# Performance work log

Hardware: AMD Instinct MI355X
Metric: run time of the kernel (lower is better)

The kernel has to match this reference:

```python
import jax, jax.numpy as jnp
import numpy as np
import math

B, T, D_MODEL, N_HEADS = 4, 2048, 1024, 16
HEAD_DIM = D_MODEL // N_HEADS


def setup_inputs() -> dict:
    key = jax.random.key(0)
    k1, k2, k3 = jax.random.split(key, 3)
    x = jax.random.normal(k1, (B, T, D_MODEL), dtype=jnp.float32)
    # torch Linear weight layout: [out_features, in_features]
    w_qkv = jax.random.normal(k2, (3 * D_MODEL, D_MODEL), dtype=jnp.float32) * (1.0 / math.sqrt(D_MODEL))
    w_out = jax.random.normal(k3, (D_MODEL, D_MODEL), dtype=jnp.float32) * (1.0 / math.sqrt(D_MODEL))
    return {"x": x, "w_qkv": w_qkv, "w_out": w_out}


def reference(x, w_qkv, w_out):
    b, t, c = x.shape
    h, d = N_HEADS, HEAD_DIM
    # qkv projection: (B,T,3C) -> (3,B,H,T,D)
    qkv = jnp.einsum('btc,fc->btf', x, w_qkv)
    qkv = qkv.reshape(b, t, 3, h, d).transpose(2, 0, 3, 1, 4)
    q, k, v = qkv[0], qkv[1], qkv[2]
    scale = 1.0 / math.sqrt(d)
    # full O(T^2) attention scores, causal masked
    scores = jnp.einsum('bhqd,bhkd->bhqk', q, k) * scale
    causal = jnp.tril(jnp.ones((t, t), dtype=bool))
    scores = jnp.where(causal[None, None, :, :], scores, jnp.float32(-jnp.inf))
    attn = jax.nn.softmax(scores, axis=-1)
    out = jnp.einsum('bhqk,bhkd->bhqd', attn, v)  # (B,H,T,D)
    out = out.transpose(0, 2, 1, 3).reshape(b, t, c)
    out = jnp.einsum('btc,oc->bto', out, w_out)
    return out
```

## Files before the change

### kernel.cpp

```cpp
#include <hip/hip_runtime.h>
#include <hip/hip_bf16.h>

#define T_SEQ 2048
#define BATCH 4
#define NH    16
#define DM    1024
#define HD    64

typedef __attribute__((ext_vector_type(4))) float  f32x4;
typedef __attribute__((ext_vector_type(8))) short  s16x8;
typedef __attribute__((ext_vector_type(4))) short  s16x4;
typedef __attribute__((ext_vector_type(4))) unsigned short u16x4;

__device__ __forceinline__ unsigned short f2b(float f) {
  union { float f; unsigned u; } v; v.f = f;
  unsigned u = v.u;
  unsigned r = 0x7fffu + ((u >> 16) & 1u);
  u += r;
  return (unsigned short)(u >> 16);
}

__device__ __forceinline__ f32x4 mfma16(s16x8 a, s16x8 b, f32x4 c) {
  return __builtin_amdgcn_mfma_f32_16x16x32_bf16(a, b, c, 0, 0, 0);
}

__device__ __forceinline__ float exp2_fast(float x) {
  float r; asm("v_exp_f32 %0, %1" : "=v"(r) : "v"(x)); return r;
}

__device__ __forceinline__ unsigned cvt_pk_bf16(float lo, float hi) {
  unsigned r; asm("v_cvt_pk_bf16_f32 %0, %1, %2" : "=v"(r) : "v"(lo), "v"(hi)); return r;
}

__global__ void cvt_all(const float* __restrict__ x, const float* __restrict__ wq,
                        const float* __restrict__ wo,
                        unsigned short* __restrict__ xb, unsigned short* __restrict__ wqb,
                        unsigned short* __restrict__ wob) {
  const int N4X = (BATCH * T_SEQ * DM) / 4;
  const int N4Q = (3 * DM * DM) / 4;
  const int N4O = (DM * DM) / 4;
  const int N4QSCALED = (DM * DM) / 4;
  int i = blockIdx.x * blockDim.x + threadIdx.x;
  int stride = gridDim.x * blockDim.x;
  for (int j = i; j < N4X + N4Q + N4O; j += stride) {
    const float* src; unsigned short* dst; int k; float scale = 1.f;
    if (j < N4X) { src = x; dst = xb; k = j; }
    else if (j < N4X + N4Q) {
      k = j - N4X; src = wq; dst = wqb;
      if (k < N4QSCALED) scale = 0.18033688011112042f;
    } else { k = j - N4X - N4Q; src = wo; dst = wob; }
    f32x4 v = ((const f32x4*)src)[k];
    s16x4 o;
    o.x = (short)f2b(v.x * scale); o.y = (short)f2b(v.y * scale);
    o.z = (short)f2b(v.z * scale); o.w = (short)f2b(v.w * scale);
    ((s16x4*)dst)[k] = o;
  }
}

template<int OUT_F32>
__global__ __launch_bounds__(256)
void gemm_bt(const unsigned short* __restrict__ A,
             const unsigned short* __restrict__ B,
             void* __restrict__ C, int M, int N, int K) {
  __shared__ unsigned short As[128 * 32];
  __shared__ unsigned short Bs[128 * 32];
  const int tid  = threadIdx.x;
  const int lane = tid & 63;
  const int w    = tid >> 6;
  const int wr   = w >> 1, wc = w & 1;
  const int lr   = lane & 15, g = lane >> 4;

  const int gx  = gridDim.x, nwg = gx * gridDim.y;
  const int bid = blockIdx.y * gx + blockIdx.x;
  const int cpx = nwg >> 3;
  const int b2  = (bid & 7) * cpx + (bid >> 3);
  const int row0 = (b2 % gx) * 128;
  const int col0 = (b2 / gx) * 128;

  const int srow = w * 16 + (lane >> 2);
  const int scol = (lane & 3) * 8;

  f32x4 acc[4][4] = {};

  for (int kt = 0; kt < K; kt += 32) {
    __syncthreads();
#pragma unroll
    for (int s = 0; s < 2; ++s) {
      const unsigned short* srcA = A + (size_t)(row0 + s * 64 + srow) * K + kt + scol;
      __builtin_amdgcn_global_load_lds((const void*)srcA, (void*)&As[(s * 64 + w * 16) * 32], 16, 0, 0);
      const unsigned short* srcB = B + (size_t)(col0 + s * 64 + srow) * K + kt + scol;
      __builtin_amdgcn_global_load_lds((const void*)srcB, (void*)&Bs[(s * 64 + w * 16) * 32], 16, 0, 0);
    }
    __syncthreads();

    s16x8 af[4], bf[4];
#pragma unroll
    for (int m = 0; m < 4; ++m)
      af[m] = *(const s16x8*)&As[(wr * 64 + m * 16 + lr) * 32 + g * 8];
#pragma unroll
    for (int n = 0; n < 4; ++n)
      bf[n] = *(const s16x8*)&Bs[(wc * 64 + n * 16 + lr) * 32 + g * 8];
#pragma unroll
    for (int m = 0; m < 4; ++m)
#pragma unroll
      for (int n = 0; n < 4; ++n)
        acc[m][n] = mfma16(af[m], bf[n], acc[m][n]);
  }

#pragma unroll
  for (int m = 0; m < 4; ++m)
#pragma unroll
    for (int n = 0; n < 4; ++n)
#pragma unroll
      for (int i = 0; i < 4; ++i) {
        int row = row0 + wr * 64 + m * 16 + g * 4 + i;
        int col = col0 + wc * 64 + n * 16 + lr;
        if (OUT_F32)
          ((float*)C)[(size_t)row * N + col] = acc[m][n][i];
        else
          ((unsigned short*)C)[(size_t)row * N + col] = f2b(acc[m][n][i]);
      }
}

__global__ __launch_bounds__(512)
void attn_kernel(const unsigned short* __restrict__ qkv,
                 unsigned short* __restrict__ out) {
  __shared__ unsigned short Ks[2][64 * 64];
  __shared__ unsigned short Vt[2][64 * 72];
  __shared__ unsigned short Ps[8][16 * 72];

  const int tid  = threadIdx.x;
  const int lane = tid & 63;
  const int w    = tid >> 6;
  const int lr   = lane & 15, g = lane >> 4;
  const int bid  = blockIdx.x;
  const int bh   = bid & 63;
  const int pi   = bid >> 6;
  const int b    = bh >> 4, h = bh & 15;
  const size_t rb = (size_t)b * T_SEQ;

  const bool grpV = (tid < 256);
  const int vd0 = (tid & 7) * 8, vr0 = (tid >> 3) * 2;
  const int t2  = tid - 256;
  const int kr0 = t2 >> 3, kc0 = t2 & 7;

#pragma unroll 1
  for (int ph = 0; ph < 2; ++ph) {
    const int qt = ph ? (15 - pi) : pi;
    const int q0 = qt * 128;
    const int qr = q0 + w * 16;
    const int qq = qr + lr;
    const int nt = 2 * qt + 2;
    const int qmax = qr + 15;

    s16x8 qf[2];
    {
      const unsigned short* qp = qkv + (rb + qq) * 3072 + h * 64;
      qf[0] = *(const s16x8*)(qp + g * 8);
      qf[1] = *(const s16x8*)(qp + 32 + g * 8);
    }

    float mI = -1e30f, lI = 0.f;
    f32x4 o[4] = {};

    s16x8 pre0, pre1;
    {
      if (grpV) {
        const unsigned short* vp = &qkv[(rb + vr0) * 3072 + 2048 + h * 64 + vd0];
        pre0 = *(const s16x8*)vp;
        pre1 = *(const s16x8*)(vp + 3072);
      } else {
        const unsigned short* kp = &qkv[(rb + kr0) * 3072 + 1024 + h * 64 + kc0 * 8];
        pre0 = *(const s16x8*)kp;
        pre1 = *(const s16x8*)(kp + 32 * 3072);
      }
    }

    for (int t = 0; t < nt; ++t) {
      const int cur = t & 1;
      if (grpV) {
#pragma unroll
        for (int jj = 0; jj < 8; ++jj) {
          int d = vd0 + jj;
          int sw = ((d ^ (d >> 3)) & 7) << 4;
          unsigned val = (unsigned)(unsigned short)pre0[jj] |
                         ((unsigned)(unsigned short)pre1[jj] << 16);
          *(unsigned*)((char*)&Vt[cur][0] + d * 144 + ((vr0 * 2) ^ sw)) = val;
        }
      } else {
        *(s16x8*)((char*)&Ks[cur][0] + kr0 * 128 + ((kc0 * 16) ^ ((kr0 & 7) << 4))) = pre0;
        int kr1 = kr0 + 32;
        *(s16x8*)((char*)&Ks[cur][0] + kr1 * 128 + ((kc0 * 16) ^ ((kr1 & 7) << 4))) = pre1;
      }
      __syncthreads();

      if (t + 1 < nt) {
        const int kv0n = (t + 1) * 64;
        if (grpV) {
          const unsigned short* vp = &qkv[(rb + kv0n + vr0) * 3072 + 2048 + h * 64 + vd0];
          pre0 = *(const s16x8*)vp;
          pre1 = *(const s16x8*)(vp + 3072);
        } else {
          const unsigned short* kp = &qkv[(rb + kv0n + kr0) * 3072 + 1024 + h * 64 + kc0 * 8];
          pre0 = *(const s16x8*)kp;
          pre1 = *(const s16x8*)(kp + 32 * 3072);
        }
      }

      const int kv0 = t * 64;
      if (kv0 <= qmax) {
        f32x4 s4[4];
        __builtin_amdgcn_s_setprio(1);
#pragma unroll
        for (int kc = 0; kc < 4; ++kc) {
          int row = kc * 16 + lr;
          const char* kbase = (const char*)&Ks[cur][0] + row * 128;
          int sw = (row & 7) << 4;
          s16x8 kf0 = *(const s16x8*)(kbase + ((g * 16) ^ sw));
          s16x8 kf1 = *(const s16x8*)(kbase + ((64 + g * 16) ^ sw));
          f32x4 s = {};
          s = mfma16(kf0, qf[0], s);
          s = mfma16(kf1, qf[1], s);
          s4[kc] = s;
        }
        __builtin_amdgcn_s_setprio(0);

        if (kv0 + 63 > qr) {
#pragma unroll
          for (int kc = 0; kc < 4; ++kc)
#pragma unroll
            for (int i = 0; i < 4; ++i) {
              int key = kv0 + kc * 16 + g * 4 + i;
              if (key > qq) s4[kc][i] = -1e30f;
            }
        }

        float mx = fmaxf(fmaxf(fmaxf(s4[0][0], s4[0][1]), fmaxf(s4[0][2], s4[0][3])),
                   fmaxf(fmaxf(fmaxf(s4[1][0], s4[1][1]), fmaxf(s4[1][2], s4[1][3])),
                   fmaxf(fmaxf(fmaxf(s4[2][0], s4[2][1]), fmaxf(s4[2][2], s4[2][3])),
                         fmaxf(fmaxf(s4[3][0], s4[3][1]), fmaxf(s4[3][2], s4[3][3])))));
        mx = fmaxf(mx, __shfl_xor(mx, 16));
        mx = fmaxf(mx, __shfl_xor(mx, 32));

        const bool defer = __all(mx - mI <= 11.5f);
        float alpha;
        if (defer) {
          alpha = 1.f;
        } else {
          float mn = fmaxf(mI, mx);
          alpha = exp2_fast(mI - mn);
          mI = mn;
        }
        float rs = 0.f;
#pragma unroll
        for (int kc = 0; kc < 4; ++kc)
#pragma unroll
          for (int i = 0; i < 4; ++i) {
            float p = exp2_fast(s4[kc][i] - mI);
            s4[kc][i] = p;
            rs += p;
          }
        rs += __shfl_xor(rs, 16);
        rs += __shfl_xor(rs, 32);
        lI = lI * alpha + rs;

        {
          char* pw = (char*)&Ps[w][0] + lr * 144;
#pragma unroll
          for (int kc = 0; kc < 4; ++kc) {
            unsigned v0 = cvt_pk_bf16(s4[kc][0], s4[kc][1]);
            unsigned v1 = cvt_pk_bf16(s4[kc][2], s4[kc][3]);
            unsigned long long pv = (unsigned long long)v0 | ((unsigned long long)v1 << 32);
            *(unsigned long long*)(pw + kc * 32 + g * 8) = pv;
          }
        }

        if (!defer) {
#pragma unroll
          for (int n = 0; n < 4; ++n)
#pragma unroll
            for (int i = 0; i < 4; ++i)
              o[n][i] *= alpha;
        }

        asm volatile("s_waitcnt lgkmcnt(0)" ::: "memory");

        __builtin_amdgcn_s_setprio(1);
#pragma unroll
        for (int kk = 0; kk < 2; ++kk) {
          s16x8 pf = *(const s16x8*)((const char*)&Ps[w][0] + lr * 144 + kk * 64 + g * 16);
#pragma unroll
          for (int n = 0; n < 4; ++n) {
            int d = n * 16 + lr;
            int sw = ((d ^ (d >> 3)) & 7) << 4;
            s16x8 vf = *(const s16x8*)((const char*)&Vt[cur][0] + d * 144 + ((kk * 64 + g * 16) ^ sw));
            o[n] = mfma16(vf, pf, o[n]);
          }
        }
        __builtin_amdgcn_s_setprio(0);
      }
    }

    float rl = 1.f / lI;
#pragma unroll
    for (int n = 0; n < 4; ++n) {
      unsigned p0 = cvt_pk_bf16(o[n][0] * rl, o[n][1] * rl);
      unsigned p1 = cvt_pk_bf16(o[n][2] * rl, o[n][3] * rl);
      unsigned long long pv = (unsigned long long)p0 | ((unsigned long long)p1 << 32);
      *(unsigned long long*)&out[(rb + qq) * 1024 + h * 64 + n * 16 + g * 4] = pv;
    }
  }
}

extern "C" void kernel_launch(void* const* d_in, const int* in_sizes, int n_in,
                              void* d_out, int out_size, void* d_ws, size_t ws_size,
                              hipStream_t stream) {
  const float* x     = (const float*)d_in[0];
  const float* w_qkv = (const float*)d_in[1];
  const float* w_out = (const float*)d_in[2];

  const size_t n_x   = (size_t)BATCH * T_SEQ * DM;
  const size_t n_wq  = (size_t)3 * DM * DM;
  const size_t n_wo  = (size_t)DM * DM;
  const size_t n_qkv = (size_t)BATCH * T_SEQ * 3 * DM;
  const size_t need  = (n_x + n_wq + n_wo + n_qkv + n_x) * 2;
  if (ws_size < need) return;

  unsigned short* xb  = (unsigned short*)d_ws;
  unsigned short* wqb = xb + n_x;
  unsigned short* wob = wqb + n_wq;
  unsigned short* qkv = wob + n_wo;
  unsigned short* att = qkv + n_qkv;

  cvt_all<<<2048, 256, 0, stream>>>(x, w_qkv, w_out, xb, wqb, wob);

  gemm_bt<0><<<dim3(64, 24), 256, 0, stream>>>(xb, wqb, qkv, BATCH * T_SEQ, 3 * DM, DM);
  attn_kernel<<<512, 512, 0, stream>>>(qkv, att);
  gemm_bt<1><<<dim3(64, 8), 256, 0, stream>>>(att, wob, d_out, BATCH * T_SEQ, DM, DM);
}
```

Before: 200.2 us.

## Replace QKV projection GEMM with 256x256-tile 8-wave pipelined direct-to-LDS kernel

Adds a new bf16 GEMM kernel for the QKV projection. It uses 256x256 output tiles, 512 threads and 128KB of double-buffered LDS. Tiles are staged with global_load_lds and an XOR swizzle, and explicit waitcnt and barrier scheduling interleaves loads, LDS reads and MFMA clusters at raised priority. The goal is more data reuse per tile and memory latency hidden behind MFMA work. In exchange it uses heavy register pressure, launches only 384 workgroups (fewer than two waves across the CUs), and its exact hand-tuned waitcnt counts are fragile.

```diff
diff --git a/kernel.cpp b/kernel.cpp
--- a/kernel.cpp
+++ b/kernel.cpp
@@ -10,7 +10,6 @@
 typedef __attribute__((ext_vector_type(4))) float  f32x4;
 typedef __attribute__((ext_vector_type(8))) short  s16x8;
 typedef __attribute__((ext_vector_type(4))) short  s16x4;
-typedef __attribute__((ext_vector_type(4))) unsigned short u16x4;
 
 __device__ __forceinline__ unsigned short f2b(float f) {
   union { float f; unsigned u; } v; v.f = f;
@@ -31,6 +30,11 @@
 __device__ __forceinline__ unsigned cvt_pk_bf16(float lo, float hi) {
   unsigned r; asm("v_cvt_pk_bf16_f32 %0, %1, %2" : "=v"(r) : "v"(lo), "v"(hi)); return r;
 }
+
+#define BAR() __builtin_amdgcn_s_barrier()
+#define SCB() __builtin_amdgcn_sched_barrier(0)
+#define LGK(n) do { asm volatile("s_waitcnt lgkmcnt(" #n ")" ::: "memory"); SCB(); } while (0)
+#define VMC(n) do { asm volatile("s_waitcnt vmcnt(" #n ")" ::: "memory"); } while (0)
 
 __global__ void cvt_all(const float* __restrict__ x, const float* __restrict__ wq,
                         const float* __restrict__ wo,
@@ -57,6 +61,150 @@
   }
 }
 
+__device__ __forceinline__ void rd4(s16x8 (&d)[4], const char* base, int rbase, int cb) {
+#pragma unroll
+  for (int j = 0; j < 4; ++j)
+    d[j] = *(const s16x8*)(base + (rbase + j * 16) * 128 + cb);
+}
+
+__device__ __forceinline__ void stage_half(const unsigned short* __restrict__ Msrc,
+                                           int rt0, int kt, char* lbase, int half,
+                                           int srow8, int c2src, int c2lin, int Kd) {
+#pragma unroll
+  for (int q = 0; q < 2; ++q) {
+    int rl = half * 128 + q * 64 + srow8;
+    const char* src = (const char*)(Msrc + (size_t)(rt0 + rl) * Kd + kt) + c2src;
+    __builtin_amdgcn_global_load_lds((const void*)src, (void*)(lbase + rl * 128 + c2lin),
+                                     16, 0, 0);
+  }
+}
+
+__device__ __forceinline__ void clust(f32x4 (&acc)[8][4], const s16x8 (&a)[4],
+                                      const s16x8 (&b)[4], int mb) {
+  __builtin_amdgcn_s_setprio(1);
+#pragma unroll
+  for (int j = 0; j < 4; ++j)
+#pragma unroll
+    for (int n = 0; n < 4; ++n)
+      acc[mb + j][n] = mfma16(a[j], b[n], acc[mb + j][n]);
+  __builtin_amdgcn_s_setprio(0);
+}
+
+__global__ __launch_bounds__(512, 2)
+void gemm8p(const unsigned short* __restrict__ A, const unsigned short* __restrict__ B,
+            unsigned short* __restrict__ C, int M, int N, int K) {
+  __shared__ char smem[131072];
+  char* A0b = smem;
+  char* A1b = smem + 32768;
+  char* B0b = smem + 65536;
+  char* B1b = smem + 98304;
+
+  const int tid = threadIdx.x;
+  const int lane = tid & 63;
+  const int w = tid >> 6;
+  const int wm = w >> 2, wn = w & 3;
+  const int lr = lane & 15, g = lane >> 4;
+
+  const int gx = gridDim.x, nwg = gx * gridDim.y;
+  const int bid = blockIdx.y * gx + blockIdx.x;
+  const int cpx = nwg >> 3;
+  const int b2 = (bid & 7) * cpx + (bid >> 3);
+  const int row0 = (b2 % gx) * 256;
+  const int col0 = (b2 / gx) * 256;
+
+  const int srow8 = tid >> 3;
+  const int c2lin = (tid & 7) * 16;
+  const int swzS = ((srow8 & 4) << 3) | ((srow8 & 8) << 1);
+  const int c2src = c2lin ^ swzS;
+
+  const int swzL = ((lr & 4) << 3) | ((lr & 8) << 1);
+  const int cs0 = (g * 16) ^ swzL;
+  const int cs1 = 64 + cs0;
+  const int rAlo = wm * 128 + lr;
+  const int rAhi = rAlo + 64;
+  const int rB = wn * 64 + lr;
+
+  f32x4 acc[8][4] = {};
+  s16x8 aP[4], aQ[4], aR[4], bP[4], bQ[4];
+
+  const int NITER = K / 128;
+  const int ktLast = K - 64;
+
+  stage_half(A, row0, 0, A0b, 0, srow8, c2src, c2lin, K);
+  stage_half(A, row0, 0, A0b, 1, srow8, c2src, c2lin, K);
+  stage_half(B, col0, 0, B0b, 0, srow8, c2src, c2lin, K);
+  stage_half(B, col0, 0, B0b, 1, srow8, c2src, c2lin, K);
+  stage_half(A, row0, 64, A1b, 0, srow8, c2src, c2lin, K);
+  VMC(2);
+  BAR();
+  rd4(aP, A0b, rAlo, cs0);
+  rd4(bP, B0b, rB, cs0);
+
+  for (int it = 0; it < NITER; ++it) {
+    const int ktO = it * 128 + 64;
+    const int kt2 = min(it * 128 + 128, ktLast);
+    const int kt3 = min(it * 128 + 192, ktLast);
+
+    rd4(aQ, A0b, rAhi, cs0);
+    stage_half(B, col0, ktO, B1b, 0, srow8, c2src, c2lin, K);
+    BAR(); LGK(4);
+    clust(acc, aP, bP, 0);
+    BAR();
+    rd4(aP, A0b, rAlo, cs1);
+    rd4(aR, A0b, rAhi, cs1);
+    rd4(bQ, B0b, rB, cs1);
+    stage_half(B, col0, ktO, B1b, 1, srow8, c2src, c2lin, K);
+    BAR(); LGK(12);
+    clust(acc, aQ, bP, 4);
+    BAR();
+    stage_half(A, row0, ktO, A1b, 1, srow8, c2src, c2lin, K);
+    BAR(); LGK(0);
+    clust(acc, aP, bQ, 0);
+    BAR();
+    stage_half(A, row0, kt2, A0b, 0, srow8, c2src, c2lin, K);
+    VMC(2);
+    BAR();
+    rd4(aP, A1b, rAlo, cs0);
+    rd4(bP, B1b, rB, cs0);
+    clust(acc, aR, bQ, 4);
+    BAR();
+    rd4(aQ, A1b, rAhi, cs0);
+    stage_half(B, col0, kt2, B0b, 0, srow8, c2src, c2lin, K);
+    BAR(); LGK(4);
+    clust(acc, aP, bP, 0);
+    BAR();
+    rd4(aP, A1b, rAlo, cs1);
+    rd4(aR, A1b, rAhi, cs1);
+    rd4(bQ, B1b, rB, cs1);
+    stage_half(B, col0, kt2, B0b, 1, srow8, c2src, c2lin, K);
+    BAR(); LGK(12);
+    clust(acc, aQ, bP, 4);
+    BAR();
+    stage_half(A, row0, kt2, A0b, 1, srow8, c2src, c2lin, K);
+    BAR(); LGK(0);
+    clust(acc, aP, bQ, 0);
+    BAR();
+    stage_half(A, row0, kt3, A1b, 0, srow8, c2src, c2lin, K);
+    VMC(2);
+    BAR();
+    rd4(aP, A0b, rAlo, cs0);
+    rd4(bP, B0b, rB, cs0);
+    clust(acc, aR, bQ, 4);
+    BAR();
+  }
+
+#pragma unroll
+  for (int m = 0; m < 8; ++m)
+#pragma unroll
+    for (int n = 0; n < 4; ++n)
+#pragma unroll
+      for (int i = 0; i < 4; ++i) {
+        int row = row0 + wm * 128 + m * 16 + g * 4 + i;
+        int col = col0 + wn * 64 + n * 16 + lr;
+        C[(size_t)row * N + col] = f2b(acc[m][n][i]);
+      }
+}
+
 template<int OUT_F32>
 __global__ __launch_bounds__(256)
 void gemm_bt(const unsigned short* __restrict__ A,
@@ -334,7 +482,7 @@
 
   cvt_all<<<2048, 256, 0, stream>>>(x, w_qkv, w_out, xb, wqb, wob);
 
-  gemm_bt<0><<<dim3(64, 24), 256, 0, stream>>>(xb, wqb, qkv, BATCH * T_SEQ, 3 * DM, DM);
+  gemm8p<<<dim3(32, 12), 512, 0, stream>>>(xb, wqb, qkv, BATCH * T_SEQ, 3 * DM, DM);
   attn_kernel<<<512, 512, 0, stream>>>(qkv, att);
   gemm_bt<1><<<dim3(64, 8), 256, 0, stream>>>(att, wob, d_out, BATCH * T_SEQ, DM, DM);
 }
```

New measurement: 199.3 us. No clear change (-0.5%).
